# Kernel optimization log

Measured on AMD Instinct MI355X. Metric: run time of the kernel, lower is better.

## Reference

```python
import jax, jax.numpy as jnp
import numpy as np

B, S, HID = 1, 1024, 4096
H, D = 32, 128
KB, NUM_SLOTS, KB_IDX = 2048, 2, 0
TOPK = 100
THETA = 10000.0
KB_SCALE = 100.0
NEG = -1e9


def _rope(x, pos):
    # x: [B,H,S,D], pos: [B,S]
    inv = 1.0 / (THETA ** (jnp.arange(0, D, 2, dtype=jnp.float32) / D))
    freqs = pos[..., None].astype(jnp.float32) * inv          # [B,S,D/2]
    emb = jnp.concatenate([freqs, freqs], -1)                  # [B,S,D]
    cos = jnp.cos(emb)[:, None]                                # [B,1,S,D]
    sin = jnp.sin(emb)[:, None]
    x1, x2 = jnp.split(x, 2, -1)
    rot = jnp.concatenate([-x2, x1], -1)
    return x * cos + rot * sin


def setup_inputs() -> dict:
    key = jax.random.key(0)
    ks = jax.random.split(key, 8)
    hidden_states = jax.random.normal(ks[0], (B, S, HID), jnp.float32)
    # standard additive causal mask (0 on allowed, large negative above diagonal)
    causal = jnp.tril(jnp.ones((S, S), bool))
    attention_mask = jnp.where(causal, 0.0, NEG).astype(jnp.float32)[None, None]
    position_ids = jnp.arange(S, dtype=jnp.int64 if jax.config.jax_enable_x64 else jnp.int32)[None].astype(jnp.int32)
    kb_keys = jax.random.normal(ks[1], (KB, NUM_SLOTS * HID), jnp.float32)
    kb_values = jax.random.normal(ks[2], (KB, NUM_SLOTS * HID), jnp.float32)
    std = 0.02
    Wq = jax.random.normal(ks[3], (HID, HID), jnp.float32) * std
    Wq2 = jax.random.normal(ks[4], (HID, HID), jnp.float32) * std
    Wk = jax.random.normal(ks[5], (HID, HID), jnp.float32) * std
    Wv = jax.random.normal(ks[6], (HID, HID), jnp.float32) * std
    Wo = jax.random.normal(ks[7], (HID, HID), jnp.float32) * std
    score_shift = jnp.zeros((H, 1), jnp.float32) - 3.0
    return dict(hidden_states=hidden_states, attention_mask=attention_mask,
                position_ids=position_ids, kb_keys=kb_keys, kb_values=kb_values,
                Wq=Wq, Wq2=Wq2, Wk=Wk, Wv=Wv, Wo=Wo, score_shift=score_shift)


def reference(hidden_states, attention_mask, position_ids, kb_keys, kb_values,
              Wq, Wq2, Wk, Wv, Wo, score_shift):
    b, s, _ = hidden_states.shape
    heads = lambda x: x.reshape(b, s, H, D).transpose(0, 2, 1, 3)
    q = heads(hidden_states @ Wq.T)
    q2 = heads(hidden_states @ Wq2.T)
    k = heads(hidden_states @ Wk.T)
    v = heads(hidden_states @ Wv.T)
    q = _rope(q, position_ids)
    k = _rope(k, position_ids)
    scale = 1.0 / jnp.sqrt(jnp.asarray(D, jnp.float32))

    # ---- KB branch (2-dim kb_kvs, layer_idx % kb_layer_frequency == 0) ----
    kbk = kb_keys.reshape(KB, NUM_SLOTS, HID)[:, KB_IDX].reshape(KB, H, D).transpose(1, 0, 2)  # [H,KB,D]
    kbv = kb_values.reshape(KB, NUM_SLOTS, HID)[:, KB_IDX].reshape(KB, H, D).transpose(1, 0, 2)
    kbk = jnp.broadcast_to(kbk[None], (b, H, KB, D))
    kbv = jnp.broadcast_to(kbv[None], (b, H, KB, D))

    # dynamic_sparsify: top-k pruning of KB entries by summed q2-scores
    aw2_full = jnp.einsum('bhqd,bhkd->bhqk', q2, kbk) * scale     # [b,H,S,KB]
    kb_scores = jax.lax.stop_gradient(aw2_full.sum((1, 2)))       # [b,KB]
    _, top_idx = jax.lax.top_k(kb_scores, TOPK)                   # [b,TOPK]
    gather = jax.vmap(lambda a, i: a[:, i])                        # [H,KB,D],[TOPK]->[H,TOPK,D]
    kbk_t = gather(kbk, top_idx)
    kbv_t = gather(kbv, top_idx)

    keys = jnp.concatenate([kbk_t, k], 2)                         # [b,H,TOPK+S,D]
    vals = jnp.concatenate([kbv_t, v], 2)

    aw = jnp.einsum('bhqd,bhkd->bhqk', q, keys) * scale           # [b,H,S,TOPK+S]

    # sep_query_head: KB logits use q2, per-head score_shift, log scale-factor correction
    aw2 = jnp.einsum('bhqd,bhkd->bhqk', q2, kbk_t) * scale        # [b,H,S,TOPK]
    aw2 = aw2 + score_shift.reshape(1, H, 1, 1)
    aw2 = aw2 - jnp.log(jnp.asarray(TOPK, jnp.float32)) + jnp.log(jnp.asarray(KB_SCALE, jnp.float32))
    aw = jnp.concatenate([aw2, aw[..., TOPK:]], -1)

    # mask: KB columns fully visible (no fully-padded rows in causal mask)
    kb_mask = jnp.zeros((b, 1, s, TOPK), attention_mask.dtype)
    mask = jnp.concatenate([kb_mask, attention_mask], -1)
    probs = jax.nn.softmax((aw + mask).astype(jnp.float32), -1).astype(q.dtype)

    out = jnp.einsum('bhqk,bhkd->bhqd', probs, vals)
    out = out.transpose(0, 2, 1, 3).reshape(b, s, HID)
    return out @ Wo.T
```

## Files before the change

kernel.cpp:

```cpp
#include <hip/hip_runtime.h>
#include <hip/hip_bf16.h>
#include <math.h>

typedef __hip_bfloat16 bf16_t;
typedef __attribute__((ext_vector_type(8))) short short8;
typedef __attribute__((ext_vector_type(4))) float f32x4;

#define S_LEN 1024
#define HID   4096
#define NH    32
#define HD    128
#define KB_N  2048
#define TOPK  100
#define SCALE 0.08838834764831845f

typedef const __attribute__((address_space(1))) void* gptr_t;
typedef __attribute__((address_space(3))) void* lptr_t;

#define VM4 asm volatile("s_waitcnt vmcnt(4)" ::: "memory")
#define VM0 asm volatile("s_waitcnt vmcnt(0)" ::: "memory")

__global__ void k0_zero(float* __restrict__ hssum) {
  int tid = threadIdx.x;
  float4 z = {0.f, 0.f, 0.f, 0.f};
  *(float4*)(hssum + tid * 4) = z;
  *(float4*)(hssum + 1024 + tid * 4) = z;
  *(float4*)(hssum + 2048 + tid * 4) = z;
  *(float4*)(hssum + 3072 + tid * 4) = z;
}

__global__ void kw_conv(const float* __restrict__ Wq, const float* __restrict__ Wq2,
                        const float* __restrict__ Wk, const float* __restrict__ Wv,
                        const float* __restrict__ Wo,
                        bf16_t* __restrict__ Wcat, bf16_t* __restrict__ Wob) {
  int w = blockIdx.y;
  const float* src = (w == 0) ? Wq : (w == 1) ? Wq2 : (w == 2) ? Wk : (w == 3) ? Wv : Wo;
  bf16_t* dst = (w < 4) ? (Wcat + (size_t)w * 16777216) : Wob;
  size_t i = ((size_t)blockIdx.x * 256 + threadIdx.x) * 4;
  float4 f = *(const float4*)(src + i);
  union { bf16_t h[4]; uint2 u; } p;
  p.h[0] = __float2bfloat16(f.x); p.h[1] = __float2bfloat16(f.y);
  p.h[2] = __float2bfloat16(f.z); p.h[3] = __float2bfloat16(f.w);
  *(uint2*)(dst + i) = p.u;
}

__global__ void k1_convert(const float* __restrict__ hs, bf16_t* __restrict__ hsb) {
  size_t i = ((size_t)blockIdx.x * 256 + threadIdx.x) * 4;
  float4 f = *(const float4*)(hs + i);
  union { bf16_t h[4]; uint2 u; } p;
  p.h[0] = __float2bfloat16(f.x); p.h[1] = __float2bfloat16(f.y);
  p.h[2] = __float2bfloat16(f.z); p.h[3] = __float2bfloat16(f.w);
  *(uint2*)(hsb + i) = p.u;
}

__global__ void k1_colsum(const float* __restrict__ hs, float* __restrict__ hssum) {
  int col = blockIdx.x * 256 + threadIdx.x;
  int r0 = blockIdx.y * 64;
  float acc = 0.f;
#pragma unroll 8
  for (int r = 0; r < 64; r++) acc += hs[(size_t)(r0 + r) * HID + col];
  atomicAdd(hssum + col, acc);
}

__global__ void k2_q2sum(const float* __restrict__ W,
                         const float* __restrict__ hssum,
                         float* __restrict__ q2sum) {
  int wave = threadIdx.x >> 6, lane = threadIdx.x & 63;
  int row = blockIdx.x * 4 + wave;
  const float4* wr = (const float4*)(W + (size_t)row * HID);
  const float4* xr = (const float4*)hssum;
  float acc = 0.f;
#pragma unroll
  for (int it = 0; it < 16; it++) {
    float4 a = wr[it * 64 + lane];
    float4 b = xr[it * 64 + lane];
    acc += a.x * b.x + a.y * b.y + a.z * b.z + a.w * b.w;
  }
#pragma unroll
  for (int off = 32; off > 0; off >>= 1) acc += __shfl_xor(acc, off, 64);
  if (lane == 0) q2sum[row] = acc;
}

__global__ void k3_kbscore(const float* __restrict__ kbk,
                           const float* __restrict__ q2sum,
                           float* __restrict__ scores) {
  int wave = threadIdx.x >> 6, lane = threadIdx.x & 63;
  int row = blockIdx.x * 4 + wave;
  const float4* kr = (const float4*)(kbk + (size_t)row * 8192);
  const float4* xr = (const float4*)q2sum;
  float acc = 0.f;
#pragma unroll
  for (int it = 0; it < 16; it++) {
    float4 a = kr[it * 64 + lane];
    float4 b = xr[it * 64 + lane];
    acc += a.x * b.x + a.y * b.y + a.z * b.z + a.w * b.w;
  }
#pragma unroll
  for (int off = 32; off > 0; off >>= 1) acc += __shfl_xor(acc, off, 64);
  if (lane == 0) scores[row] = acc * SCALE;
}

__global__ void k4_topk(const float* __restrict__ scores, int* __restrict__ tidx) {
  int lane = threadIdx.x;
  float v[32];
#pragma unroll
  for (int i = 0; i < 32; i++) v[i] = scores[i * 64 + lane];
  for (int t = 0; t < TOPK; t++) {
    float bm = -INFINITY; int bi = 0x7fffffff;
#pragma unroll
    for (int i = 0; i < 32; i++) {
      if (v[i] > bm) { bm = v[i]; bi = i * 64 + lane; }
    }
#pragma unroll
    for (int off = 32; off > 0; off >>= 1) {
      float ov = __shfl_xor(bm, off, 64);
      int   oi = __shfl_xor(bi, off, 64);
      if (ov > bm || (ov == bm && oi < bi)) { bm = ov; bi = oi; }
    }
    if (lane == 0) tidx[t] = bi;
    if ((bi & 63) == lane) {
      int slot = bi >> 6;
#pragma unroll
      for (int i = 0; i < 32; i++) if (i == slot) v[i] = -INFINITY;
    }
  }
}

__global__ void k5_gather(const float* __restrict__ kbk, const float* __restrict__ kbv,
                          const int* __restrict__ tidx,
                          bf16_t* __restrict__ kbkt, bf16_t* __restrict__ kbvt) {
  int j = blockIdx.x;
  int tid = threadIdx.x;
  if (j < TOPK) {
    size_t src = (size_t)tidx[j] * 8192;
#pragma unroll
    for (int r = 0; r < 4; r++) {
      int i = (tid + r * 256) * 4;
      float4 a = *(const float4*)(kbk + src + i);
      float4 b = *(const float4*)(kbv + src + i);
      union { bf16_t h[4]; uint2 u; } pa, pb;
      pa.h[0] = __float2bfloat16(a.x); pa.h[1] = __float2bfloat16(a.y);
      pa.h[2] = __float2bfloat16(a.z); pa.h[3] = __float2bfloat16(a.w);
      pb.h[0] = __float2bfloat16(b.x); pb.h[1] = __float2bfloat16(b.y);
      pb.h[2] = __float2bfloat16(b.z); pb.h[3] = __float2bfloat16(b.w);
      *(uint2*)(kbkt + (size_t)j * HID + i) = pa.u;
      *(uint2*)(kbvt + (size_t)j * HID + i) = pb.u;
    }
  } else {
    uint2 z; z.x = 0u; z.y = 0u;
#pragma unroll
    for (int r = 0; r < 4; r++) {
      int i = (tid + r * 256) * 4;
      *(uint2*)(kbkt + (size_t)j * HID + i) = z;
      *(uint2*)(kbvt + (size_t)j * HID + i) = z;
    }
  }
}

__global__ __launch_bounds__(512, 2) void gemm_proj(
    const bf16_t* __restrict__ A, const bf16_t* __restrict__ B,
    void* O0, void* O1, void* O2, void* O3) {
  __shared__ __attribute__((aligned(16))) bf16_t sm[4 * 16384];
  const int tid  = threadIdx.x;
  const int wave = tid >> 6, lane = tid & 63;
  const int lrow = lane & 15, quad = lane >> 4;
  const int wr = wave >> 2, wc = wave & 3;
  const int bm = blockIdx.y * 256;
  const int bn = blockIdx.x * 256;
  const int srow = tid >> 2;
  const int lc   = (tid & 3) ^ ((srow >> 1) & 3);
  const int pc   = quad ^ ((lrow >> 1) & 3);

  const bf16_t* aS = A + (size_t)(bm + srow) * 4096 + lc * 8;
  const bf16_t* bS = B + (size_t)(bn + srow) * 4096 + lc * 8;
  bf16_t* const lw = sm + wave * 512;

  f32x4 acc[8][4];
  const f32x4 zero4 = {0.f, 0.f, 0.f, 0.f};
#pragma unroll
  for (int i = 0; i < 8; i++)
#pragma unroll
    for (int j = 0; j < 4; j++) acc[i][j] = zero4;

  auto STAGE = [&](int tt) {
    bf16_t* l = lw + (tt & 3) * 16384;
    const bf16_t* ga = aS + tt * 32;
    const bf16_t* gb = bS + tt * 32;
    __builtin_amdgcn_global_load_lds((gptr_t)ga,             (lptr_t)l,           16, 0, 0);
    __builtin_amdgcn_global_load_lds((gptr_t)(ga + 524288),  (lptr_t)(l + 4096),  16, 0, 0);
    __builtin_amdgcn_global_load_lds((gptr_t)gb,             (lptr_t)(l + 8192),  16, 0, 0);
    __builtin_amdgcn_global_load_lds((gptr_t)(gb + 524288),  (lptr_t)(l + 12288), 16, 0, 0);
  };

  short8 fa0[4], fb0[4], fa1[4], fb1[4], afB[4];

  auto body = [&](int t, short8 (&FAC)[4], short8 (&FBC)[4],
                  short8 (&FAN)[4], short8 (&FBN)[4],
                  bool pf, bool stg, int vmn, bool barr) {
    const bf16_t* Ab = sm + (t & 3) * 16384 + (wr * 128 + lrow) * 32 + pc * 8;
    if (stg) STAGE(t + 3);
#pragma unroll
    for (int i = 0; i < 4; i++) afB[i] = *(const short8*)(Ab + (i + 4) * 512);
    __builtin_amdgcn_s_setprio(1);
#pragma unroll
    for (int i = 0; i < 4; i++)
#pragma unroll
      for (int j = 0; j < 4; j++)
        acc[i][j] = __builtin_amdgcn_mfma_f32_16x16x32_bf16(FAC[i], FBC[j], acc[i][j], 0, 0, 0);
    __builtin_amdgcn_s_setprio(0);
    if (pf) {
      const bf16_t* An = sm + ((t + 1) & 3) * 16384 + (wr * 128 + lrow) * 32 + pc * 8;
      const bf16_t* Bn = sm + ((t + 1) & 3) * 16384 + 8192 + (wc * 64 + lrow) * 32 + pc * 8;
#pragma unroll
      for (int j = 0; j < 4; j++) FBN[j] = *(const short8*)(Bn + j * 512);
#pragma unroll
      for (int i = 0; i < 4; i++) FAN[i] = *(const short8*)(An + i * 512);
    }
    __builtin_amdgcn_s_setprio(1);
#pragma unroll
    for (int i = 0; i < 4; i++)
#pragma unroll
      for (int j = 0; j < 4; j++)
        acc[i + 4][j] = __builtin_amdgcn_mfma_f32_16x16x32_bf16(afB[i], FBC[j], acc[i + 4][j], 0, 0, 0);
    __builtin_amdgcn_s_setprio(0);
    if (vmn == 4) { VM4; }
    else if (vmn == 0) { VM0; }
    if (barr) __builtin_amdgcn_s_barrier();
  };

  STAGE(0); STAGE(1); STAGE(2);
  VM4;
  __builtin_amdgcn_s_barrier();
  {
    const bf16_t* Ab = sm + (wr * 128 + lrow) * 32 + pc * 8;
    const bf16_t* Bb = sm + 8192 + (wc * 64 + lrow) * 32 + pc * 8;
#pragma unroll
    for (int j = 0; j < 4; j++) fb0[j] = *(const short8*)(Bb + j * 512);
#pragma unroll
    for (int i = 0; i < 4; i++) fa0[i] = *(const short8*)(Ab + i * 512);
  }

  for (int t = 0; t < 124; t += 2) {
    body(t,     fa0, fb0, fa1, fb1, true, true, 4, true);
    body(t + 1, fa1, fb1, fa0, fb0, true, true, 4, true);
  }
  body(124, fa0, fb0, fa1, fb1, true,  true,  4, true);
  body(125, fa1, fb1, fa0, fb0, true,  false, 0, true);
  body(126, fa0, fb0, fa1, fb1, true,  false, -1, false);
  body(127, fa1, fb1, fa0, fb0, false, false, -1, false);

  bf16_t* dst = (bf16_t*)((bn >> 12) == 0 ? O0 : (bn >> 12) == 1 ? O1
                        : (bn >> 12) == 2 ? O2 : O3);
  const int nb = bn & 4095;
#pragma unroll
  for (int i = 0; i < 8; i++)
#pragma unroll
    for (int j = 0; j < 4; j++)
#pragma unroll
      for (int r = 0; r < 4; r++) {
        int m = bm + wr * 128 + i * 16 + quad * 4 + r;
        int n = nb + wc * 64 + j * 16 + lrow;
        dst[(size_t)m * 4096 + n] = __float2bfloat16(acc[i][j][r]);
      }
}

__global__ __launch_bounds__(512, 2) void gemm_wo(
    const bf16_t* __restrict__ A, const bf16_t* __restrict__ B,
    float* __restrict__ out) {
  __shared__ __attribute__((aligned(16))) bf16_t sm[4 * 16384];
  const int tid  = threadIdx.x;
  const int wave = tid >> 6, lane = tid & 63;
  const int lrow = lane & 15, quad = lane >> 4;
  const int wrr = wave >> 2, wcc = wave & 3;
  const int bm = blockIdx.y * 128;
  const int bn = blockIdx.x * 128;
  const int srow8 = lane >> 3;
  const int lcw   = (lane & 7) ^ srow8;
  const int grp   = (wave & 3) * 32;
  const bf16_t* wS = ((wave < 4) ? A + (size_t)(bm + grp + srow8) * 4096
                                 : B + (size_t)(bn + grp + srow8) * 4096) + lcw * 8;
  bf16_t* const lw = sm + (wave < 4 ? 0 : 8192) + grp * 64;
  const int pcw0 = ((quad)     ^ (lrow & 7)) * 8;
  const int pcw1 = ((4 + quad) ^ (lrow & 7)) * 8;

  f32x4 acc[4][2];
  const f32x4 zero4 = {0.f, 0.f, 0.f, 0.f};
#pragma unroll
  for (int i = 0; i < 4; i++)
#pragma unroll
    for (int j = 0; j < 2; j++) acc[i][j] = zero4;

  auto STAGE = [&](int tt) {
    bf16_t* l = lw + (tt & 3) * 16384;
    const bf16_t* g = wS + tt * 64;
    __builtin_amdgcn_global_load_lds((gptr_t)g,              (lptr_t)l,           16, 0, 0);
    __builtin_amdgcn_global_load_lds((gptr_t)(g + 32768),    (lptr_t)(l + 512),   16, 0, 0);
    __builtin_amdgcn_global_load_lds((gptr_t)(g + 65536),    (lptr_t)(l + 1024),  16, 0, 0);
    __builtin_amdgcn_global_load_lds((gptr_t)(g + 98304),    (lptr_t)(l + 1536),  16, 0, 0);
  };

  short8 ga0[8], gb0[4], ga1[8], gb1[4];

  auto rdfrag = [&](int t, short8 (&GA)[8], short8 (&GB)[4]) {
    const bf16_t* An = sm + (t & 3) * 16384;
    const bf16_t* Bn = An + 8192;
#pragma unroll
    for (int n = 0; n < 2; n++) {
      int row = wcc * 32 + n * 16 + lrow;
      GB[n * 2]     = *(const short8*)(Bn + row * 64 + pcw0);
      GB[n * 2 + 1] = *(const short8*)(Bn + row * 64 + pcw1);
    }
#pragma unroll
    for (int m = 0; m < 4; m++) {
      int row = wrr * 64 + m * 16 + lrow;
      GA[m * 2]     = *(const short8*)(An + row * 64 + pcw0);
      GA[m * 2 + 1] = *(const short8*)(An + row * 64 + pcw1);
    }
  };

  auto body = [&](int t, short8 (&GA)[8], short8 (&GB)[4],
                  short8 (&NA)[8], short8 (&NB)[4],
                  bool pf, bool stg, int vmn, bool barr) {
    if (stg) STAGE(t + 3);
    if (pf) rdfrag(t + 1, NA, NB);
    __builtin_amdgcn_s_setprio(1);
#pragma unroll
    for (int kk = 0; kk < 2; kk++)
#pragma unroll
      for (int m = 0; m < 4; m++)
#pragma unroll
        for (int n = 0; n < 2; n++)
          acc[m][n] = __builtin_amdgcn_mfma_f32_16x16x32_bf16(
              GA[m * 2 + kk], GB[n * 2 + kk], acc[m][n], 0, 0, 0);
    __builtin_amdgcn_s_setprio(0);
    if (vmn == 4) { VM4; }
    else if (vmn == 0) { VM0; }
    if (barr) __builtin_amdgcn_s_barrier();
  };

  STAGE(0); STAGE(1); STAGE(2);
  VM4;
  __builtin_amdgcn_s_barrier();
  rdfrag(0, ga0, gb0);

  for (int t = 0; t < 60; t += 2) {
    body(t,     ga0, gb0, ga1, gb1, true, true, 4, true);
    body(t + 1, ga1, gb1, ga0, gb0, true, true, 4, true);
  }
  body(60, ga0, gb0, ga1, gb1, true,  true,  4, true);
  body(61, ga1, gb1, ga0, gb0, true,  false, 0, true);
  body(62, ga0, gb0, ga1, gb1, true,  false, -1, false);
  body(63, ga1, gb1, ga0, gb0, false, false, -1, false);

#pragma unroll
  for (int m = 0; m < 4; m++)
#pragma unroll
    for (int n = 0; n < 2; n++)
#pragma unroll
      for (int r = 0; r < 4; r++) {
        int row = bm + wrr * 64 + m * 16 + quad * 4 + r;
        int col = bn + wcc * 32 + n * 16 + lrow;
        out[(size_t)row * 4096 + col] = acc[m][n][r];
      }
}

template<int OUT_BF16>
__global__ __launch_bounds__(256) void gemm_bt(
    const bf16_t* __restrict__ A,
    const float* __restrict__ B0, const float* __restrict__ B1,
    const float* __restrict__ B2, const float* __restrict__ B3,
    void* C0, void* C1, void* C2, void* C3) {
  const int z = blockIdx.z;
  const float* __restrict__ B = (z == 0) ? B0 : (z == 1) ? B1 : (z == 2) ? B2 : B3;
  void* Cv = (z == 0) ? C0 : (z == 1) ? C1 : (z == 2) ? C2 : C3;
  __shared__ bf16_t As[128][40];
  __shared__ bf16_t Bs[128][40];
  const int tid = threadIdx.x;
  const int bm = blockIdx.y * 128, bn = blockIdx.x * 128;
  const int wave = tid >> 6, lane = tid & 63;
  const int wr = wave >> 1, wc = wave & 1;
  const int lrow = lane & 15, quad = lane >> 4;
  f32x4 acc[4][4];
  const f32x4 zero4 = {0.f, 0.f, 0.f, 0.f};
#pragma unroll
  for (int i = 0; i < 4; i++)
#pragma unroll
    for (int j = 0; j < 4; j++) acc[i][j] = zero4;
  const int arow = tid >> 2, ach = tid & 3;
  const int brow = tid >> 3, bch = tid & 7;
  for (int k0 = 0; k0 < 4096; k0 += 32) {
    __syncthreads();
#pragma unroll
    for (int r = 0; r < 2; r++) {
      int row = arow + r * 64;
      uint4 val = *(const uint4*)(A + (size_t)(bm + row) * 4096 + k0 + ach * 8);
      *(uint4*)(&As[row][ach * 8]) = val;
    }
#pragma unroll
    for (int r = 0; r < 4; r++) {
      int row = brow + r * 32;
      float4 f = *(const float4*)(B + (size_t)(bn + row) * 4096 + k0 + bch * 4);
      union { bf16_t h[4]; uint2 u; } p;
      p.h[0] = __float2bfloat16(f.x); p.h[1] = __float2bfloat16(f.y);
      p.h[2] = __float2bfloat16(f.z); p.h[3] = __float2bfloat16(f.w);
      *(uint2*)(&Bs[row][bch * 4]) = p.u;
    }
    __syncthreads();
    short8 af[4], bfr[4];
#pragma unroll
    for (int i = 0; i < 4; i++)
      af[i] = *(const short8*)(&As[wr * 64 + i * 16 + lrow][quad * 8]);
#pragma unroll
    for (int j = 0; j < 4; j++)
      bfr[j] = *(const short8*)(&Bs[wc * 64 + j * 16 + lrow][quad * 8]);
#pragma unroll
    for (int i = 0; i < 4; i++)
#pragma unroll
      for (int j = 0; j < 4; j++)
        acc[i][j] = __builtin_amdgcn_mfma_f32_16x16x32_bf16(af[i], bfr[j], acc[i][j], 0, 0, 0);
  }
#pragma unroll
  for (int i = 0; i < 4; i++)
#pragma unroll
    for (int j = 0; j < 4; j++)
#pragma unroll
      for (int r = 0; r < 4; r++) {
        int m = bm + wr * 64 + i * 16 + quad * 4 + r;
        int n = bn + wc * 64 + j * 16 + lrow;
        if (OUT_BF16)
          ((bf16_t*)Cv)[(size_t)m * 4096 + n] = __float2bfloat16(acc[i][j][r]);
        else
          ((float*)Cv)[(size_t)m * 4096 + n] = acc[i][j][r];
      }
}

__global__ void k7_rope(bf16_t* __restrict__ q, bf16_t* __restrict__ k,
                        const int* __restrict__ pos_ids) {
  int t = blockIdx.x * 256 + threadIdx.x;
  int d = t & 63;
  int h = (t >> 6) & 31;
  int s = t >> 11;
  float pos = (float)pos_ids[s];
  float inv = exp2f(-(float)d * 0.20762050593046f);
  float ang = pos * inv;
  float c = cosf(ang), si = sinf(ang);
  size_t i1 = (size_t)s * HID + h * HD + d;
  size_t i2 = i1 + 64;
  float a1 = __bfloat162float(q[i1]), a2 = __bfloat162float(q[i2]);
  q[i1] = __float2bfloat16(a1 * c - a2 * si);
  q[i2] = __float2bfloat16(a2 * c + a1 * si);
  float b1 = __bfloat162float(k[i1]), b2 = __bfloat162float(k[i2]);
  k[i1] = __float2bfloat16(b1 * c - b2 * si);
  k[i2] = __float2bfloat16(b2 * c + b1 * si);
}

#define FA_PAD 136
__global__ __launch_bounds__(256) void k8_flash(
    const bf16_t* __restrict__ qg, const bf16_t* __restrict__ q2g,
    const bf16_t* __restrict__ kg, const bf16_t* __restrict__ vg,
    const bf16_t* __restrict__ kbkt, const bf16_t* __restrict__ kbvt,
    const float* __restrict__ shift_p,
    bf16_t* __restrict__ outb) {
  __shared__ bf16_t KV[128][FA_PAD];
  __shared__ bf16_t Ps[4][16][FA_PAD];
  int qt = 15 - (int)blockIdx.x;
  int h = blockIdx.y;
  int q0 = qt * 64;
  int tid = threadIdx.x;
  int wave = tid >> 6, lane = tid & 63;
  int lrow = lane & 15, quad = lane >> 4;

  short8 qf[4], q2f[4];
  {
    const size_t base = (size_t)(q0 + wave * 16 + lrow) * HID + h * HD;
#pragma unroll
    for (int kc = 0; kc < 4; kc++) {
      qf[kc]  = *(const short8*)(qg  + base + kc * 32 + quad * 8);
      q2f[kc] = *(const short8*)(q2g + base + kc * 32 + quad * 8);
    }
  }
  const f32x4 zero4 = {0.f, 0.f, 0.f, 0.f};
  f32x4 O[8];
#pragma unroll
  for (int df = 0; df < 8; df++) O[df] = zero4;
  float m_i[4], l_i[4];
#pragma unroll
  for (int r = 0; r < 4; r++) { m_i[r] = -INFINITY; l_i[r] = 0.f; }
  float shift = shift_p[h];

  int nt = (q0 + 63) / 128 + 1;
  for (int tile = -1; tile < nt; tile++) {
    const bf16_t* ksrc = (tile < 0) ? (kbkt + h * HD)
                                    : (kg + (size_t)tile * 128 * HID + h * HD);
    const bf16_t* vsrc = (tile < 0) ? (kbvt + h * HD)
                                    : (vg + (size_t)tile * 128 * HID + h * HD);
    __syncthreads();
    {
      int rbase = tid >> 4, ch = tid & 15;
#pragma unroll
      for (int rr = 0; rr < 8; rr++) {
        int row = rr * 16 + rbase;
        uint4 val = *(const uint4*)(ksrc + (size_t)row * HID + ch * 8);
        *(uint4*)(&KV[row][ch * 8]) = val;
      }
    }
    __syncthreads();
    f32x4 Sv[8];
#pragma unroll
    for (int jf = 0; jf < 8; jf++) {
      short8 kf[4];
#pragma unroll
      for (int kc = 0; kc < 4; kc++)
        kf[kc] = *(const short8*)(&KV[jf * 16 + lrow][kc * 32 + quad * 8]);
      f32x4 s = zero4;
      if (tile < 0) {
#pragma unroll
        for (int kc = 0; kc < 4; kc++)
          s = __builtin_amdgcn_mfma_f32_16x16x32_bf16(q2f[kc], kf[kc], s, 0, 0, 0);
      } else {
#pragma unroll
        for (int kc = 0; kc < 4; kc++)
          s = __builtin_amdgcn_mfma_f32_16x16x32_bf16(qf[kc], kf[kc], s, 0, 0, 0);
      }
      Sv[jf] = s;
    }
#pragma unroll
    for (int jf = 0; jf < 8; jf++)
#pragma unroll
      for (int r = 0; r < 4; r++) {
        float val = Sv[jf][r] * SCALE;
        if (tile < 0) {
          val += shift;
          int col = jf * 16 + lrow;
          if (col >= TOPK) val = -1e30f;
        } else {
          int srow = q0 + wave * 16 + quad * 4 + r;
          int tcol = tile * 128 + jf * 16 + lrow;
          if (tcol > srow) val -= 1e9f;
        }
        Sv[jf][r] = val;
      }
    float alpha[4];
#pragma unroll
    for (int r = 0; r < 4; r++) {
      float tm = Sv[0][r];
#pragma unroll
      for (int jf = 1; jf < 8; jf++) tm = fmaxf(tm, Sv[jf][r]);
#pragma unroll
      for (int off = 1; off < 16; off <<= 1) tm = fmaxf(tm, __shfl_xor(tm, off, 64));
      float mn = fmaxf(m_i[r], tm);
      alpha[r] = __expf(m_i[r] - mn);
      m_i[r] = mn;
    }
    float rsum[4] = {0.f, 0.f, 0.f, 0.f};
#pragma unroll
    for (int jf = 0; jf < 8; jf++)
#pragma unroll
      for (int r = 0; r < 4; r++) {
        float p = __expf(Sv[jf][r] - m_i[r]);
        Sv[jf][r] = p;
        rsum[r] += p;
      }
#pragma unroll
    for (int r = 0; r < 4; r++) {
#pragma unroll
      for (int off = 1; off < 16; off <<= 1) rsum[r] += __shfl_xor(rsum[r], off, 64);
      l_i[r] = l_i[r] * alpha[r] + rsum[r];
    }
#pragma unroll
    for (int jf = 0; jf < 8; jf++)
#pragma unroll
      for (int r = 0; r < 4; r++)
        Ps[wave][quad * 4 + r][jf * 16 + lrow] = __float2bfloat16(Sv[jf][r]);
#pragma unroll
    for (int df = 0; df < 8; df++)
#pragma unroll
      for (int r = 0; r < 4; r++) O[df][r] *= alpha[r];
    __syncthreads();
    {
      int rbase = tid >> 4, ch = tid & 15;
#pragma unroll
      for (int rr = 0; rr < 8; rr++) {
        int t = rr * 16 + rbase;
        union { uint4 u; bf16_t hx[8]; } vv;
        vv.u = *(const uint4*)(vsrc + (size_t)t * HID + ch * 8);
        int cs = ((t >> 3) ^ ch) & 15;
        int tl = t & 7;
#pragma unroll
        for (int e = 0; e < 8; e++)
          KV[ch * 8 + e][cs * 8 + tl] = vv.hx[e];
      }
    }
    __syncthreads();
    short8 pf[4];
#pragma unroll
    for (int kc = 0; kc < 4; kc++)
      pf[kc] = *(const short8*)(&Ps[wave][lrow][kc * 32 + quad * 8]);
#pragma unroll
    for (int df = 0; df < 8; df++) {
      int d = df * 16 + lrow;
      int sw = (d >> 3) & 15;
#pragma unroll
      for (int kc = 0; kc < 4; kc++) {
        short8 vf = *(const short8*)(&KV[d][(((kc * 4 + quad) ^ sw) & 15) * 8]);
        O[df] = __builtin_amdgcn_mfma_f32_16x16x32_bf16(pf[kc], vf, O[df], 0, 0, 0);
      }
    }
  }
#pragma unroll
  for (int df = 0; df < 8; df++)
#pragma unroll
    for (int r = 0; r < 4; r++) {
      int srow = q0 + wave * 16 + quad * 4 + r;
      float val = O[df][r] / l_i[r];
      outb[(size_t)srow * HID + h * HD + df * 16 + lrow] = __float2bfloat16(val);
    }
}

extern "C" void kernel_launch(void* const* d_in, const int* in_sizes, int n_in,
                              void* d_out, int out_size, void* d_ws, size_t ws_size,
                              hipStream_t stream) {
  const float* hs    = (const float*)d_in[0];
  const int*   pos   = (const int*)d_in[2];
  const float* kbk   = (const float*)d_in[3];
  const float* kbv   = (const float*)d_in[4];
  const float* Wq    = (const float*)d_in[5];
  const float* Wq2   = (const float*)d_in[6];
  const float* Wk    = (const float*)d_in[7];
  const float* Wv    = (const float*)d_in[8];
  const float* Wo    = (const float*)d_in[9];
  const float* shift = (const float*)d_in[10];
  float* out = (float*)d_out;

  char* ws = (char*)d_ws;
  const size_t MB8 = 8388608;
  bf16_t* qb    = (bf16_t*)(ws);
  bf16_t* q2b   = (bf16_t*)(ws + MB8);
  bf16_t* kbuf  = (bf16_t*)(ws + 2 * MB8);
  bf16_t* vbuf  = (bf16_t*)(ws + 3 * MB8);
  bf16_t* hsb   = (bf16_t*)(ws + 4 * MB8);
  bf16_t* kbkt  = (bf16_t*)(ws + 5 * MB8);
  bf16_t* kbvt  = (bf16_t*)(ws + 5 * MB8 + 1048576);
  float*  hssum = (float*)(ws + 5 * MB8 + 2 * 1048576);
  float*  q2s   = (float*)(ws + 5 * MB8 + 2 * 1048576 + 16384);
  float*  scr   = (float*)(ws + 5 * MB8 + 2 * 1048576 + 32768);
  int*    tidx  = (int*)(ws + 5 * MB8 + 2 * 1048576 + 40960);
  bf16_t* attnb = hsb;
  const size_t WCAT_OFF = 48ull * 1048576;
  bf16_t* Wcat = (bf16_t*)(ws + WCAT_OFF);
  bf16_t* Wob  = (bf16_t*)(ws + WCAT_OFF + 134217728);
  const size_t WS_NEED = WCAT_OFF + 134217728 + 33554432;
  const bool big_ws = (ws_size >= WS_NEED);

  k0_zero<<<dim3(1), dim3(256), 0, stream>>>(hssum);
  if (big_ws)
    kw_conv<<<dim3(16384, 5), dim3(256), 0, stream>>>(Wq, Wq2, Wk, Wv, Wo, Wcat, Wob);
  k1_convert<<<dim3(4096), dim3(256), 0, stream>>>(hs, hsb);
  k1_colsum<<<dim3(16, 16), dim3(256), 0, stream>>>(hs, hssum);
  k2_q2sum<<<dim3(1024), dim3(256), 0, stream>>>(Wq2, hssum, q2s);
  k3_kbscore<<<dim3(512), dim3(256), 0, stream>>>(kbk, q2s, scr);
  k4_topk<<<dim3(1), dim3(64), 0, stream>>>(scr, tidx);
  k5_gather<<<dim3(128), dim3(256), 0, stream>>>(kbk, kbv, tidx, kbkt, kbvt);

  if (big_ws) {
    gemm_proj<<<dim3(64, 4), dim3(512), 0, stream>>>(
        hsb, Wcat, (void*)qb, (void*)q2b, (void*)kbuf, (void*)vbuf);
  } else {
    gemm_bt<1><<<dim3(32, 8, 4), dim3(256), 0, stream>>>(
        hsb, Wq, Wq2, Wk, Wv, (void*)qb, (void*)q2b, (void*)kbuf, (void*)vbuf);
  }
  k7_rope<<<dim3(8192), dim3(256), 0, stream>>>(qb, kbuf, pos);
  k8_flash<<<dim3(16, 32), dim3(256), 0, stream>>>(
      qb, q2b, kbuf, vbuf, kbkt, kbvt, shift, attnb);
  if (big_ws) {
    gemm_wo<<<dim3(32, 8), dim3(512), 0, stream>>>(attnb, Wob, out);
  } else {
    gemm_bt<0><<<dim3(32, 8, 1), dim3(256), 0, stream>>>(
        attnb, Wo, Wo, Wo, Wo, (void*)out, (void*)out, (void*)out, (void*)out);
  }
}
```

Before: 758.7 us.

## Load A operand fragments directly from global into registers in projection GEMM

The projection GEMM stops staging the A tile through LDS. Each wave now reads its A fragments straight from global memory into registers, prefetched one k-step ahead, and only the B tile goes through the LDS ring, which halves LDS use per stage. Wait counts are retuned (vmcnt 10) to cover the extra outstanding register loads. This removes LDS traffic and shared-memory footprint for A, at the cost of uncoalesced, duplicated global reads, since the four waves sharing an A row block each fetch it themselves, and higher register pressure.

```diff
diff --git a/kernel.cpp b/kernel.cpp
--- a/kernel.cpp
+++ b/kernel.cpp
@@ -17,8 +17,9 @@
 typedef const __attribute__((address_space(1))) void* gptr_t;
 typedef __attribute__((address_space(3))) void* lptr_t;
 
-#define VM4 asm volatile("s_waitcnt vmcnt(4)" ::: "memory")
-#define VM0 asm volatile("s_waitcnt vmcnt(0)" ::: "memory")
+#define VM10 asm volatile("s_waitcnt vmcnt(10)" ::: "memory")
+#define VM4  asm volatile("s_waitcnt vmcnt(4)" ::: "memory")
+#define VM0  asm volatile("s_waitcnt vmcnt(0)" ::: "memory")
 
 __global__ void k0_zero(float* __restrict__ hssum) {
   int tid = threadIdx.x;
@@ -160,20 +161,21 @@
 __global__ __launch_bounds__(512, 2) void gemm_proj(
     const bf16_t* __restrict__ A, const bf16_t* __restrict__ B,
     void* O0, void* O1, void* O2, void* O3) {
-  __shared__ __attribute__((aligned(16))) bf16_t sm[4 * 16384];
+  __shared__ __attribute__((aligned(16))) bf16_t sm[4 * 8192];
   const int tid  = threadIdx.x;
   const int wave = tid >> 6, lane = tid & 63;
   const int lrow = lane & 15, quad = lane >> 4;
   const int wr = wave >> 2, wc = wave & 3;
   const int bm = blockIdx.y * 256;
   const int bn = blockIdx.x * 256;
-  const int srow = tid >> 2;
-  const int lc   = (tid & 3) ^ ((srow >> 1) & 3);
-  const int pc   = quad ^ ((lrow >> 1) & 3);
-
-  const bf16_t* aS = A + (size_t)(bm + srow) * 4096 + lc * 8;
-  const bf16_t* bS = B + (size_t)(bn + srow) * 4096 + lc * 8;
-  bf16_t* const lw = sm + wave * 512;
+  const int pc = quad ^ ((lrow >> 1) & 3);
+
+  const int r0  = wave * 32 + (lane >> 2);
+  const int lc0 = (lane & 3) ^ ((r0 >> 1) & 3);
+  const bf16_t* bS0 = B + (size_t)(bn + r0) * 4096 + lc0 * 8;
+  const bf16_t* bS1 = B + (size_t)(bn + r0 + 16) * 4096 + lc0 * 8;
+
+  const bf16_t* aP = A + (size_t)(bm + wr * 128 + lrow) * 4096 + quad * 8;
 
   f32x4 acc[8][4];
   const f32x4 zero4 = {0.f, 0.f, 0.f, 0.f};
@@ -183,24 +185,28 @@
     for (int j = 0; j < 4; j++) acc[i][j] = zero4;
 
   auto STAGE = [&](int tt) {
-    bf16_t* l = lw + (tt & 3) * 16384;
-    const bf16_t* ga = aS + tt * 32;
-    const bf16_t* gb = bS + tt * 32;
-    __builtin_amdgcn_global_load_lds((gptr_t)ga,             (lptr_t)l,           16, 0, 0);
-    __builtin_amdgcn_global_load_lds((gptr_t)(ga + 524288),  (lptr_t)(l + 4096),  16, 0, 0);
-    __builtin_amdgcn_global_load_lds((gptr_t)gb,             (lptr_t)(l + 8192),  16, 0, 0);
-    __builtin_amdgcn_global_load_lds((gptr_t)(gb + 524288),  (lptr_t)(l + 12288), 16, 0, 0);
+    bf16_t* l = sm + (tt & 3) * 8192 + wave * 1024;
+    __builtin_amdgcn_global_load_lds((gptr_t)(bS0 + tt * 32), (lptr_t)l,         16, 0, 0);
+    __builtin_amdgcn_global_load_lds((gptr_t)(bS1 + tt * 32), (lptr_t)(l + 512), 16, 0, 0);
   };
 
-  short8 fa0[4], fb0[4], fa1[4], fb1[4], afB[4];
+  short8 fa0[4], fb0[4], fa1[4], fb1[4];
 
   auto body = [&](int t, short8 (&FAC)[4], short8 (&FBC)[4],
                   short8 (&FAN)[4], short8 (&FBN)[4],
-                  bool pf, bool stg, int vmn, bool barr) {
-    const bf16_t* Ab = sm + (t & 3) * 16384 + (wr * 128 + lrow) * 32 + pc * 8;
+                  bool pfA, bool pfB, bool stg, int vmn, bool barr) {
+    if (pfA) {
+      const bf16_t* apn = aP + (size_t)(t + 1) * 32;
+#pragma unroll
+      for (int i = 0; i < 4; i++) FAN[i] = *(const short8*)(apn + (size_t)i * 65536);
+    }
+    short8 fam[4];
+    {
+      const bf16_t* apc = aP + (size_t)t * 32;
+#pragma unroll
+      for (int i = 0; i < 4; i++) fam[i] = *(const short8*)(apc + (size_t)(i + 4) * 65536);
+    }
     if (stg) STAGE(t + 3);
-#pragma unroll
-    for (int i = 0; i < 4; i++) afB[i] = *(const short8*)(Ab + (i + 4) * 512);
     __builtin_amdgcn_s_setprio(1);
 #pragma unroll
     for (int i = 0; i < 4; i++)
@@ -208,46 +214,41 @@
       for (int j = 0; j < 4; j++)
         acc[i][j] = __builtin_amdgcn_mfma_f32_16x16x32_bf16(FAC[i], FBC[j], acc[i][j], 0, 0, 0);
     __builtin_amdgcn_s_setprio(0);
-    if (pf) {
-      const bf16_t* An = sm + ((t + 1) & 3) * 16384 + (wr * 128 + lrow) * 32 + pc * 8;
-      const bf16_t* Bn = sm + ((t + 1) & 3) * 16384 + 8192 + (wc * 64 + lrow) * 32 + pc * 8;
-#pragma unroll
-      for (int j = 0; j < 4; j++) FBN[j] = *(const short8*)(Bn + j * 512);
-#pragma unroll
-      for (int i = 0; i < 4; i++) FAN[i] = *(const short8*)(An + i * 512);
+    if (pfB) {
+      const bf16_t* bb = sm + ((t + 1) & 3) * 8192;
+#pragma unroll
+      for (int j = 0; j < 4; j++)
+        FBN[j] = *(const short8*)(bb + (wc * 64 + j * 16 + lrow) * 32 + pc * 8);
     }
     __builtin_amdgcn_s_setprio(1);
 #pragma unroll
     for (int i = 0; i < 4; i++)
 #pragma unroll
       for (int j = 0; j < 4; j++)
-        acc[i + 4][j] = __builtin_amdgcn_mfma_f32_16x16x32_bf16(afB[i], FBC[j], acc[i + 4][j], 0, 0, 0);
+        acc[i + 4][j] = __builtin_amdgcn_mfma_f32_16x16x32_bf16(fam[i], FBC[j], acc[i + 4][j], 0, 0, 0);
     __builtin_amdgcn_s_setprio(0);
-    if (vmn == 4) { VM4; }
+    if (vmn == 10) { VM10; }
     else if (vmn == 0) { VM0; }
     if (barr) __builtin_amdgcn_s_barrier();
   };
 
   STAGE(0); STAGE(1); STAGE(2);
-  VM4;
+#pragma unroll
+  for (int i = 0; i < 4; i++) fa0[i] = *(const short8*)(aP + (size_t)i * 65536);
+  VM0;
   __builtin_amdgcn_s_barrier();
-  {
-    const bf16_t* Ab = sm + (wr * 128 + lrow) * 32 + pc * 8;
-    const bf16_t* Bb = sm + 8192 + (wc * 64 + lrow) * 32 + pc * 8;
-#pragma unroll
-    for (int j = 0; j < 4; j++) fb0[j] = *(const short8*)(Bb + j * 512);
-#pragma unroll
-    for (int i = 0; i < 4; i++) fa0[i] = *(const short8*)(Ab + i * 512);
-  }
+#pragma unroll
+  for (int j = 0; j < 4; j++)
+    fb0[j] = *(const short8*)(sm + (wc * 64 + j * 16 + lrow) * 32 + pc * 8);
 
   for (int t = 0; t < 124; t += 2) {
-    body(t,     fa0, fb0, fa1, fb1, true, true, 4, true);
-    body(t + 1, fa1, fb1, fa0, fb0, true, true, 4, true);
-  }
-  body(124, fa0, fb0, fa1, fb1, true,  true,  4, true);
-  body(125, fa1, fb1, fa0, fb0, true,  false, 0, true);
-  body(126, fa0, fb0, fa1, fb1, true,  false, -1, false);
-  body(127, fa1, fb1, fa0, fb0, false, false, -1, false);
+    body(t,     fa0, fb0, fa1, fb1, true, true, true, 10, true);
+    body(t + 1, fa1, fb1, fa0, fb0, true, true, true, 10, true);
+  }
+  body(124, fa0, fb0, fa1, fb1, true,  true,  true,  10, true);
+  body(125, fa1, fb1, fa0, fb0, true,  true,  false, 0,  true);
+  body(126, fa0, fb0, fa1, fb1, true,  true,  false, 0,  true);
+  body(127, fa1, fb1, fa0, fb0, false, false, false, -1, false);
 
   bf16_t* dst = (bf16_t*)((bn >> 12) == 0 ? O0 : (bn >> 12) == 1 ? O1
                         : (bn >> 12) == 2 ? O2 : O3);
```

Measured after the change: 968.9 us. +27.7%, slower.
